# Performance work log

Hardware: AMD Instinct MI355X
Metric: run time of the kernel (lower is better)

Reference implementation:

```python
import jax, jax.numpy as jnp
import numpy as np

B, C_IN, T = 8, 1024, 4096
VQ_C, CODEBOOK, DS = 1024, 2048, 2


def setup_inputs() -> dict:
    key = jax.random.key(0)
    ks = jax.random.split(key, 6)
    return {
        "x": jax.random.normal(ks[0], (B, C_IN, T), jnp.float32),
        "x_mask": jnp.ones((B, 1, T), jnp.float32),
        "w_in": jax.random.normal(ks[1], (VQ_C, C_IN, DS), jnp.float32) * 0.02,
        "b_in": jnp.zeros((VQ_C,), jnp.float32),
        "embed": jax.random.normal(ks[2], (CODEBOOK, VQ_C), jnp.float32),
        "w_out": jax.random.normal(ks[3], (C_IN, VQ_C), jnp.float32) * 0.02,
        "b_out": jnp.zeros((C_IN,), jnp.float32),
    }


def reference(x, x_mask, w_in, b_in, embed, w_out, b_out):
    x_len = x.shape[2]
    ds = w_in.shape[-1]
    pad = (-x_len) % ds  # static under jit
    if pad:
        x = jnp.pad(x, ((0, 0), (0, 0), (0, pad)))
        x_mask = jnp.pad(x_mask, ((0, 0), (0, 0), (0, pad)))
    b, cin, tp = x.shape
    # conv_in: Conv1d(k=ds, stride=ds) == non-overlapping window contraction
    h = jnp.einsum('bcls,ocs->bol', x.reshape(b, cin, tp // ds, ds), w_in) + b_in[None, :, None]  # [B, D, L]
    tokens = h.transpose(0, 2, 1)  # [B, L, D]
    # euclidean codebook: ||t - e||^2 expanded (stable for argmin)
    d2 = (jnp.sum(tokens * tokens, -1, keepdims=True)
          - 2.0 * jnp.einsum('bld,nd->bln', tokens, embed)
          + jnp.sum(embed * embed, -1)[None, None, :])  # [B, L, N]
    idx = jnp.argmin(d2, axis=-1)  # [B, L]
    q = embed[idx]  # gather -> [B, L, D]
    # commitment loss (training-mode math; EMA codebook -> embed not a grad path)
    commit_loss = jnp.mean((jax.lax.stop_gradient(q) - tokens) ** 2)
    # straight-through estimator
    q_st = tokens + jax.lax.stop_gradient(q - tokens)
    q_cf = q_st.transpose(0, 2, 1)  # [B, D, L]
    # conv_out: nearest upsample x ds, then 1x1 conv
    up = jnp.repeat(q_cf, ds, axis=2)  # [B, D, Tp]
    out = jnp.einsum('bct,oc->bot', up, w_out) + b_out[None, :, None]
    out = out * x_mask
    return out[:, :, :x_len], commit_loss
```

## Files before the change

### kernel.cpp

```cpp
#include <hip/hip_runtime.h>

typedef _Float16 half8 __attribute__((ext_vector_type(8)));
typedef float f32x4 __attribute__((ext_vector_type(4)));

static constexpr int D = 1024;
static constexpr int NCODE = 2048;
static constexpr int MTOK = 16384;
static constexpr int KIN = 2048;
static constexpr int TLEN = 4096;
static constexpr int CAP = 2048;
#define TAU 0.4f

__device__ __forceinline__ void gload16(const void* g, void* l) {
  __builtin_amdgcn_global_load_lds(
      (const __attribute__((address_space(1))) void*)g,
      (__attribute__((address_space(3))) void*)l, 16, 0, 0);
}

#define SBAR()   asm volatile("s_barrier" ::: "memory")
#define WAITV6() asm volatile("s_waitcnt vmcnt(6)" ::: "memory")
#define WAITV4() asm volatile("s_waitcnt vmcnt(4)" ::: "memory")
#define WAITV3() asm volatile("s_waitcnt vmcnt(3)" ::: "memory")
#define WAITV0() asm volatile("s_waitcnt vmcnt(0)" ::: "memory")

__device__ __forceinline__ float key_to_f32(unsigned u) {
  unsigned bits = (u & 0x80000000u) ? (u & 0x7FFFFFFFu) : ~u;
  return __uint_as_float(bits);
}
__device__ __forceinline__ unsigned f32_to_key(float f) {
  unsigned ub = __float_as_uint(f);
  return (ub & 0x80000000u) ? ~ub : (ub | 0x80000000u);
}

__global__ __launch_bounds__(256) void k_pack_x(const float* __restrict__ x,
                                                _Float16* __restrict__ xh,
                                                _Float16* __restrict__ xl) {
  __shared__ float lds[32][65];
  const int tt0 = blockIdx.x * 64;
  const int cc0 = blockIdx.y * 32;
  const int b = blockIdx.z;
  const float* xb = x + ((size_t)b * D + cc0) * TLEN + tt0;
#pragma unroll
  for (int i = 0; i < 8; ++i) {
    int idx = threadIdx.x + i * 256;
    lds[idx >> 6][idx & 63] = xb[(size_t)(idx >> 6) * TLEN + (idx & 63)];
  }
  __syncthreads();
  const size_t mrow0 = (size_t)b * 2048 + (tt0 >> 1);
#pragma unroll
  for (int i = 0; i < 8; ++i) {
    int idx = threadIdx.x + i * 256;
    int r = idx >> 6, kk = idx & 63;
    float v = lds[kk >> 1][2 * r + (kk & 1)];
    _Float16 h = (_Float16)v;
    size_t off = (mrow0 + r) * (size_t)KIN + (size_t)cc0 * 2 + kk;
    xh[off] = h;
    xl[off] = (_Float16)(v - (float)h);
  }
}

__global__ __launch_bounds__(256) void k_split(const float* __restrict__ s,
                                               _Float16* __restrict__ hi,
                                               _Float16* __restrict__ lo, int n) {
  int i = blockIdx.x * 256 + threadIdx.x;
  if (i < n) {
    float v = s[i];
    _Float16 h = (_Float16)v;
    hi[i] = h;
    lo[i] = (_Float16)(v - (float)h);
  }
}

__global__ __launch_bounds__(256) void k_tohalf(const float* __restrict__ s,
                                                _Float16* __restrict__ hi, int n) {
  int i = blockIdx.x * 256 + threadIdx.x;
  if (i < n) hi[i] = (_Float16)s[i];
}

__global__ __launch_bounds__(256) void k_e2(const float* __restrict__ embed,
                                            float* __restrict__ e2c) {
  int row = blockIdx.x * 4 + (threadIdx.x >> 6);
  int lane = threadIdx.x & 63;
  const float* er = embed + (size_t)row * D;
  double s = 0.0;
  for (int i = lane; i < D; i += 64) { double v = er[i]; s += v * v; }
#pragma unroll
  for (int mk = 1; mk < 64; mk <<= 1) s += __shfl_xor(s, mk, 64);
  if (lane == 0) e2c[row] = (float)(s - 1024.0);
}

template <int KDIM, int LOG_GX>
__global__ __launch_bounds__(512, 2) void k_gemm_tok3(
    const _Float16* __restrict__ Ah_, const _Float16* __restrict__ Al_,
    const _Float16* __restrict__ Bh_, const _Float16* __restrict__ Bl_,
    const float* __restrict__ vec,
    _Float16* __restrict__ outh, _Float16* __restrict__ outl,
    float* __restrict__ t2) {
  __shared__ _Float16 lds[3 * 24576];
  const int nwg = gridDim.x;
  const int bid = blockIdx.x;
  const int q = nwg >> 3;
  const int b2 = (bid & 7) * q + (bid >> 3);
  const int n0 = (b2 & ((1 << LOG_GX) - 1)) * 128;
  const int m0 = (b2 >> LOG_GX) * 256;

  const int tid = threadIdx.x, lane = tid & 63, w = tid >> 6;
  const int wr = w >> 1, wc = w & 1, lr = lane & 15, lk = lane >> 4;
  constexpr int NT = KDIM / 32;

  const int cswz8 = (((lane & 3) ^ ((lane >> 3) & 3))) * 8;
  const int rswz8 = (lk ^ ((lr >> 1) & 3)) * 8;

  f32x4 acc[4][4] = {};
  half8 ahA[4], bhA[4], ahB[4], bhB[4], al[4], bl[4];

  auto stageA2 = [&](const _Float16* __restrict__ src, int k0, char* regionBase) {
    int slot0 = w * 64 + lane;
    gload16(src + (size_t)(m0 + (slot0 >> 2)) * KDIM + k0 + cswz8,
            regionBase + w * 1024);
    int slot1 = slot0 + 512;
    gload16(src + (size_t)(m0 + (slot1 >> 2)) * KDIM + k0 + cswz8,
            regionBase + w * 1024 + 8192);
  };
  auto stageB2 = [&](int k0, char* stageBase) {
    int slot = w * 64 + lane;
    size_t go = (size_t)(n0 + (slot >> 2)) * KDIM + k0 + cswz8;
    gload16(Bh_ + go, stageBase + 32768 + w * 1024);
    gload16(Bl_ + go, stageBase + 40960 + w * 1024);
  };
  auto stageAll = [&](int t, int c) {
    char* sb = (char*)lds + c * 49152;
    stageA2(Ah_, t * 32, sb);
    stageA2(Al_, t * 32, sb + 16384);
    stageB2(t * 32, sb);
  };

  int c0 = 0, c1 = 1, c2 = 2;
  stageAll(0, 0);
  stageAll(1, 1);
  WAITV6();
  SBAR();
#pragma unroll
  for (int f = 0; f < 4; ++f) {
    ahA[f] = *(const half8*)(lds + (wr * 64 + f * 16 + lr) * 32 + rswz8);
    bhA[f] = *(const half8*)(lds + 16384 + (wc * 64 + f * 16 + lr) * 32 + rswz8);
  }

  auto tile_body = [&](int t, half8 (&ahC)[4], half8 (&bhC)[4],
                       half8 (&ahN)[4], half8 (&bhN)[4]) {
    const _Float16* sb = lds + c0 * 24576;
    char* dstb = (char*)lds + c2 * 49152;
    const bool st = (t + 2) < NT;
    const int ks = (t + 2) * 32;

#pragma unroll
    for (int f = 0; f < 4; ++f)
      bl[f] = *(const half8*)(sb + 20480 + (wc * 64 + f * 16 + lr) * 32 + rswz8);
    if (st) stageA2(Ah_, ks, dstb);
    SBAR();
    __builtin_amdgcn_s_setprio(1);
#pragma unroll
    for (int fm = 0; fm < 4; ++fm)
#pragma unroll
      for (int fn = 0; fn < 4; ++fn)
        acc[fm][fn] = __builtin_amdgcn_mfma_f32_16x16x32_f16(ahC[fm], bhC[fn], acc[fm][fn], 0, 0, 0);
    __builtin_amdgcn_s_setprio(0);
    SBAR();

#pragma unroll
    for (int f = 0; f < 4; ++f)
      al[f] = *(const half8*)(sb + 8192 + (wr * 64 + f * 16 + lr) * 32 + rswz8);
    if (st) stageA2(Al_, ks, dstb + 16384);
    WAITV4();
    SBAR();
    __builtin_amdgcn_s_setprio(1);
#pragma unroll
    for (int fm = 0; fm < 4; ++fm)
#pragma unroll
      for (int fn = 0; fn < 4; ++fn)
        acc[fm][fn] = __builtin_amdgcn_mfma_f32_16x16x32_f16(ahC[fm], bl[fn], acc[fm][fn], 0, 0, 0);
    __builtin_amdgcn_s_setprio(0);
    SBAR();

    if (t + 1 < NT) {
      const _Float16* sb1 = lds + c1 * 24576;
#pragma unroll
      for (int f = 0; f < 4; ++f) {
        ahN[f] = *(const half8*)(sb1 + (wr * 64 + f * 16 + lr) * 32 + rswz8);
        bhN[f] = *(const half8*)(sb1 + 16384 + (wc * 64 + f * 16 + lr) * 32 + rswz8);
      }
    }
    if (st) stageB2(ks, dstb);
    SBAR();
    __builtin_amdgcn_s_setprio(1);
#pragma unroll
    for (int fm = 0; fm < 4; ++fm)
#pragma unroll
      for (int fn = 0; fn < 4; ++fn)
        acc[fm][fn] = __builtin_amdgcn_mfma_f32_16x16x32_f16(al[fm], bhC[fn], acc[fm][fn], 0, 0, 0);
    __builtin_amdgcn_s_setprio(0);
    if (st) { WAITV6(); } else if (t + 1 < NT) { WAITV0(); }
    SBAR();

    int tmp = c0; c0 = c1; c1 = c2; c2 = tmp;
  };

  for (int tt = 0; tt < NT; tt += 2) {
    tile_body(tt,     ahA, bhA, ahB, bhB);
    tile_body(tt + 1, ahB, bhB, ahA, bhA);
  }

#pragma unroll
  for (int fm = 0; fm < 4; ++fm) {
#pragma unroll
    for (int j = 0; j < 4; ++j) {
      int row = wr * 64 + fm * 16 + lk * 4 + j;
      size_t m = (size_t)m0 + row;
      float v2 = 0.f;
#pragma unroll
      for (int fn = 0; fn < 4; ++fn) {
        int col = n0 + wc * 64 + fn * 16 + lr;
        float v = acc[fm][fn][j] + vec[col];
        v2 += v * v;
        _Float16 h = (_Float16)v;
        outh[m * D + col] = h;
        outl[m * D + col] = (_Float16)(v - (float)h);
      }
#pragma unroll
      for (int mk = 1; mk < 16; mk <<= 1) v2 += __shfl_xor(v2, mk, 64);
      if (lr == 0) atomicAdd(&t2[m], v2);
    }
  }
}

__global__ __launch_bounds__(512, 4) void k_score1(
    const _Float16* __restrict__ Ah_, const _Float16* __restrict__ Bh_,
    const float* __restrict__ e2c,
    unsigned long long* __restrict__ skKey, float* __restrict__ skSnd) {
  __shared__ _Float16 lds[3 * 12288];
  const int nwg = gridDim.x, bid = blockIdx.x, q = nwg >> 3;
  const int b2 = (bid & 7) * q + (bid >> 3);
  const int nb = b2 & 15;
  const int n0 = nb * 128, m0 = (b2 >> 4) * 256;
  const int tid = threadIdx.x, lane = tid & 63, w = tid >> 6;
  const int wr = w >> 1, wc = w & 1, lr = lane & 15, lk = lane >> 4;
  constexpr int NT = D / 32;
  const int cswz8 = (((lane & 3) ^ ((lane >> 3) & 3))) * 8;
  const int rswz8 = (lk ^ ((lr >> 1) & 3)) * 8;

  f32x4 acc[4][4] = {};

  auto stage = [&](int t, int c) {
    char* sb = (char*)lds + c * 24576;
    const int k0 = t * 32;
    int slot0 = w * 64 + lane;
    gload16(Ah_ + (size_t)(m0 + (slot0 >> 2)) * D + k0 + cswz8, sb + w * 1024);
    int slot1 = slot0 + 512;
    gload16(Ah_ + (size_t)(m0 + (slot1 >> 2)) * D + k0 + cswz8, sb + w * 1024 + 8192);
    gload16(Bh_ + (size_t)(n0 + (slot0 >> 2)) * D + k0 + cswz8, sb + 16384 + w * 1024);
  };

  stage(0, 0);
  stage(1, 1);
  WAITV3();
  SBAR();

  int c0 = 0, c1 = 1, c2 = 2;
  for (int t = 0; t < NT; ++t) {
    const _Float16* sb = lds + c0 * 12288;
    half8 ah[4], bh[4];
#pragma unroll
    for (int f = 0; f < 4; ++f) {
      ah[f] = *(const half8*)(sb + (wr * 64 + f * 16 + lr) * 32 + rswz8);
      bh[f] = *(const half8*)(sb + 8192 + (wc * 64 + f * 16 + lr) * 32 + rswz8);
    }
    const bool st = (t + 2) < NT;
    if (st) stage(t + 2, c2);
    SBAR();
    __builtin_amdgcn_s_setprio(1);
#pragma unroll
    for (int fm = 0; fm < 4; ++fm)
#pragma unroll
      for (int fn = 0; fn < 4; ++fn)
        acc[fm][fn] = __builtin_amdgcn_mfma_f32_16x16x32_f16(ah[fm], bh[fn], acc[fm][fn], 0, 0, 0);
    __builtin_amdgcn_s_setprio(0);
    if (st) { WAITV3(); } else if (t + 1 < NT) { WAITV0(); }
    SBAR();
    int tmp = c0; c0 = c1; c1 = c2; c2 = tmp;
  }

#pragma unroll
  for (int fm = 0; fm < 4; ++fm) {
#pragma unroll
    for (int j = 0; j < 4; ++j) {
      int row = wr * 64 + fm * 16 + lk * 4 + j;
      size_t m = (size_t)m0 + row;
      float b1 = 3.4e38f, bb2 = 3.4e38f;
      int i1 = 0x7FFFFFFF;
#pragma unroll
      for (int fn = 0; fn < 4; ++fn) {
        int col = n0 + wc * 64 + fn * 16 + lr;
        float mv = e2c[col] - 2.0f * acc[fm][fn][j];
        if (mv < b1) { bb2 = b1; b1 = mv; i1 = col; }
        else if (mv < bb2) { bb2 = mv; }
      }
#pragma unroll
      for (int mk = 1; mk < 16; mk <<= 1) {
        float ob1 = __shfl_xor(b1, mk, 64);
        float ob2 = __shfl_xor(bb2, mk, 64);
        int oi = __shfl_xor(i1, mk, 64);
        if (ob1 < b1) { bb2 = fminf(b1, ob2); b1 = ob1; i1 = oi; }
        else { bb2 = fminf(bb2, ob1); }
      }
      if (lr == 0) {
        unsigned long long key = ((unsigned long long)f32_to_key(b1) << 32) | (unsigned)i1;
        skKey[m * 32 + nb * 2 + wc] = key;
        skSnd[m * 32 + nb * 2 + wc] = bb2;
      }
    }
  }
}

__global__ __launch_bounds__(256) void k_flag(const unsigned long long* __restrict__ skKey,
                                              const float* __restrict__ skSnd,
                                              unsigned long long* __restrict__ keys,
                                              int* __restrict__ list, int* __restrict__ counter) {
  int m = blockIdx.x * 256 + threadIdx.x;
  unsigned long long best = ~0ull;
  int bsl = 0;
#pragma unroll
  for (int sl = 0; sl < 32; ++sl) {
    unsigned long long k = skKey[(size_t)m * 32 + sl];
    if (k < best) { best = k; bsl = sl; }
  }
  float b1 = key_to_f32((unsigned)(best >> 32));
  float second = skSnd[(size_t)m * 32 + bsl];
#pragma unroll
  for (int sl = 0; sl < 32; ++sl) {
    if (sl != bsl) second = fminf(second, key_to_f32((unsigned)(skKey[(size_t)m * 32 + sl] >> 32)));
  }
  keys[m] = best;
  if (second - b1 < TAU) {
    int p = atomicAdd(counter, 1);
    if (p < CAP) list[p] = m;
  }
}

__global__ __launch_bounds__(256) void k_rescore(
    const _Float16* __restrict__ tokh, const _Float16* __restrict__ tokl,
    const _Float16* __restrict__ eh, const _Float16* __restrict__ el,
    const float* __restrict__ e2c, const int* __restrict__ list,
    const int* __restrict__ counter,
    unsigned long long* __restrict__ keys2) {
  const int count = min(counter[0], CAP);
  const int m0 = blockIdx.y * 128;
  if (m0 >= count) return;
  __shared__ _Float16 sAh[128 * 32], sAl[128 * 32], sBh[128 * 32], sBl[128 * 32];
  const int n0 = blockIdx.x * 128;
  const int tid = threadIdx.x, lane = tid & 63, w = tid >> 6;
  const int wr = w >> 1, wc = w & 1, lr = lane & 15, lk = lane >> 4;
  f32x4 acc[4][4] = {};

  const int g0 = w * 128 + lane, g1 = g0 + 64;
  const int rA0 = g0 >> 2, cA0 = g0 & 3, rA1 = g1 >> 2, cA1 = g1 & 3;
  const int lb0 = (w * 128) * 16, lb1 = (w * 128 + 64) * 16;
  const int tk0 = list[m0 + rA0], tk1 = list[m0 + rA1];

  for (int kt = 0; kt < D / 32; ++kt) {
    const int k0 = kt * 32;
    gload16(tokh + (size_t)tk0 * D + k0 + cA0 * 8, (char*)sAh + lb0);
    gload16(tokh + (size_t)tk1 * D + k0 + cA1 * 8, (char*)sAh + lb1);
    gload16(tokl + (size_t)tk0 * D + k0 + cA0 * 8, (char*)sAl + lb0);
    gload16(tokl + (size_t)tk1 * D + k0 + cA1 * 8, (char*)sAl + lb1);
    gload16(eh + (size_t)(n0 + rA0) * D + k0 + cA0 * 8, (char*)sBh + lb0);
    gload16(eh + (size_t)(n0 + rA1) * D + k0 + cA1 * 8, (char*)sBh + lb1);
    gload16(el + (size_t)(n0 + rA0) * D + k0 + cA0 * 8, (char*)sBl + lb0);
    gload16(el + (size_t)(n0 + rA1) * D + k0 + cA1 * 8, (char*)sBl + lb1);
    __syncthreads();
    half8 ah[4], al2[4], bh[4], bl2[4];
#pragma unroll
    for (int f = 0; f < 4; ++f) {
      ah[f]  = *(const half8*)(sAh + (wr * 64 + f * 16 + lr) * 32 + lk * 8);
      al2[f] = *(const half8*)(sAl + (wr * 64 + f * 16 + lr) * 32 + lk * 8);
      bh[f]  = *(const half8*)(sBh + (wc * 64 + f * 16 + lr) * 32 + lk * 8);
      bl2[f] = *(const half8*)(sBl + (wc * 64 + f * 16 + lr) * 32 + lk * 8);
    }
#pragma unroll
    for (int fm = 0; fm < 4; ++fm)
#pragma unroll
      for (int fn = 0; fn < 4; ++fn) {
        acc[fm][fn] = __builtin_amdgcn_mfma_f32_16x16x32_f16(ah[fm], bh[fn], acc[fm][fn], 0, 0, 0);
        acc[fm][fn] = __builtin_amdgcn_mfma_f32_16x16x32_f16(ah[fm], bl2[fn], acc[fm][fn], 0, 0, 0);
        acc[fm][fn] = __builtin_amdgcn_mfma_f32_16x16x32_f16(al2[fm], bh[fn], acc[fm][fn], 0, 0, 0);
      }
    __syncthreads();
  }
#pragma unroll
  for (int fm = 0; fm < 4; ++fm) {
#pragma unroll
    for (int j = 0; j < 4; ++j) {
      int row = wr * 64 + fm * 16 + lk * 4 + j;
      if (m0 + row >= count) continue;
      int tm = list[m0 + row];
      float best = 3.4e38f;
      int bidx = 0x7FFFFFFF;
#pragma unroll
      for (int fn = 0; fn < 4; ++fn) {
        int col = n0 + wc * 64 + fn * 16 + lr;
        float mv = e2c[col] - 2.0f * acc[fm][fn][j];
        if (mv < best) { best = mv; bidx = col; }
      }
#pragma unroll
      for (int mk = 1; mk < 16; mk <<= 1) {
        float ob = __shfl_xor(best, mk, 64);
        int oi = __shfl_xor(bidx, mk, 64);
        if (ob < best || (ob == best && oi < bidx)) { best = ob; bidx = oi; }
      }
      if (lr == 0) {
        unsigned long long key = ((unsigned long long)f32_to_key(best) << 32) | (unsigned)bidx;
        atomicMin(&keys2[tm], key);
      }
    }
  }
}

__global__ __launch_bounds__(256) void k_merge(unsigned long long* __restrict__ keys,
                                               const unsigned long long* __restrict__ keys2) {
  int m = blockIdx.x * 256 + threadIdx.x;
  unsigned long long k2 = keys2[m];
  if (k2 != ~0ull) keys[m] = k2;
}

__global__ __launch_bounds__(256) void k_gemm_out(
    const _Float16* __restrict__ eh, const unsigned long long* __restrict__ keys,
    const _Float16* __restrict__ woh, const float* __restrict__ b_out,
    const float* __restrict__ mask, float* __restrict__ out) {
  __shared__ _Float16 sA[128 * 32], sB[128 * 32];
  __shared__ float sC[32 * 129];
  const int n0 = blockIdx.x * 128, m0 = blockIdx.y * 128;
  const int tid = threadIdx.x, lane = tid & 63, w = tid >> 6;
  const int wr = w >> 1, wc = w & 1, lr = lane & 15, lk = lane >> 4;
  f32x4 acc[4][4] = {};

  const int g0 = w * 128 + lane, g1 = g0 + 64;
  const int rA0 = g0 >> 2, cA0 = g0 & 3, rA1 = g1 >> 2, cA1 = g1 & 3;
  const int lb0 = (w * 128) * 16, lb1 = (w * 128 + 64) * 16;
  const unsigned i0 = (unsigned)(keys[m0 + rA0] & 0xFFFFFFFFull);
  const unsigned i1 = (unsigned)(keys[m0 + rA1] & 0xFFFFFFFFull);
  const _Float16* srcA0 = eh + (size_t)i0 * D + cA0 * 8;
  const _Float16* srcA1 = eh + (size_t)i1 * D + cA1 * 8;

  for (int kt = 0; kt < D / 32; ++kt) {
    const int k0 = kt * 32;
    gload16(srcA0 + k0, (char*)sA + lb0);
    gload16(srcA1 + k0, (char*)sA + lb1);
    gload16(woh + (size_t)(n0 + rA0) * D + k0 + cA0 * 8, (char*)sB + lb0);
    gload16(woh + (size_t)(n0 + rA1) * D + k0 + cA1 * 8, (char*)sB + lb1);
    __syncthreads();
    half8 a[4], b[4];
#pragma unroll
    for (int f = 0; f < 4; ++f) {
      a[f] = *(const half8*)(sA + (wr * 64 + f * 16 + lr) * 32 + lk * 8);
      b[f] = *(const half8*)(sB + (wc * 64 + f * 16 + lr) * 32 + lk * 8);
    }
#pragma unroll
    for (int fm = 0; fm < 4; ++fm)
#pragma unroll
      for (int fn = 0; fn < 4; ++fn)
        acc[fm][fn] = __builtin_amdgcn_mfma_f32_16x16x32_f16(a[fm], b[fn], acc[fm][fn], 0, 0, 0);
    __syncthreads();
  }
  for (int ch = 0; ch < 4; ++ch) {
    __syncthreads();
    if (wr == (ch >> 1)) {
      int fb = (ch & 1) * 2;
#pragma unroll
      for (int f2 = 0; f2 < 2; ++f2) {
        int fm = fb + f2;
#pragma unroll
        for (int fn = 0; fn < 4; ++fn)
#pragma unroll
          for (int j = 0; j < 4; ++j) {
            int lrow = f2 * 16 + lk * 4 + j;
            int col = wc * 64 + fn * 16 + lr;
            sC[lrow * 129 + col] = acc[fm][fn][j] + b_out[n0 + col];
          }
      }
    }
    __syncthreads();
    const int mbase = m0 + ch * 32;
    const int b = mbase >> 11;
    const int l0 = mbase & 2047;
    const float mval = mask[(size_t)b * TLEN + 2 * l0 + lane];
    for (int oo = 0; oo < 32; ++oo) {
      int ocol = w * 32 + oo;
      float v = sC[(lane >> 1) * 129 + ocol];
      out[((size_t)(b * D + n0 + ocol)) * TLEN + 2 * l0 + lane] = v * mval;
    }
  }
}

__global__ __launch_bounds__(256) void k_loss(const unsigned long long* __restrict__ keys,
                                              const float* __restrict__ t2,
                                              double* __restrict__ acc) {
  int m = blockIdx.x * 256 + threadIdx.x;
  unsigned long long k = keys[m];
  float mval = key_to_f32((unsigned)(k >> 32));
  double c = (double)mval + 1024.0 + (double)t2[m];
#pragma unroll
  for (int mk = 1; mk < 64; mk <<= 1) c += __shfl_xor(c, mk, 64);
  __shared__ double part[4];
  if ((threadIdx.x & 63) == 0) part[threadIdx.x >> 6] = c;
  __syncthreads();
  if (threadIdx.x == 0) atomicAdd(acc, part[0] + part[1] + part[2] + part[3]);
}

__global__ void k_finalize(const double* __restrict__ acc, float* __restrict__ dst) {
  if (threadIdx.x == 0 && blockIdx.x == 0) *dst = (float)(*acc * (1.0 / 16777216.0));
}

extern "C" void kernel_launch(void* const* d_in, const int* in_sizes, int n_in,
                              void* d_out, int out_size, void* d_ws, size_t ws_size,
                              hipStream_t stream) {
  (void)in_sizes; (void)n_in; (void)out_size;
  const float* x      = (const float*)d_in[0];
  const float* xmask  = (const float*)d_in[1];
  const float* w_in   = (const float*)d_in[2];
  const float* b_in   = (const float*)d_in[3];
  const float* embed  = (const float*)d_in[4];
  const float* w_out  = (const float*)d_in[5];
  const float* b_out  = (const float*)d_in[6];
  float* out = (float*)d_out;

  _Float16* xh = (_Float16*)d_out;
  _Float16* xl = xh + (size_t)MTOK * KIN;

  char* p = (char*)d_ws;
  auto take = [&](size_t sz) { char* r = p; p += (sz + 255) & ~(size_t)255; return r; };
  _Float16* wh   = (_Float16*)take((size_t)D * KIN * 2);
  _Float16* wl   = (_Float16*)take((size_t)D * KIN * 2);
  _Float16* eh   = (_Float16*)take((size_t)NCODE * D * 2);
  _Float16* el   = (_Float16*)take((size_t)NCODE * D * 2);
  _Float16* woh  = (_Float16*)take((size_t)D * D * 2);
  float* e2c     = (float*)take((size_t)NCODE * 4);
  _Float16* tokh = (_Float16*)take((size_t)MTOK * D * 2);
  _Float16* tokl = (_Float16*)take((size_t)MTOK * D * 2);
  float* t2      = (float*)take((size_t)MTOK * 4);
  unsigned long long* keys  = (unsigned long long*)take((size_t)MTOK * 8);
  unsigned long long* keys2 = (unsigned long long*)take((size_t)MTOK * 8);
  unsigned long long* skKey = (unsigned long long*)take((size_t)MTOK * 32 * 8);
  float* skSnd   = (float*)take((size_t)MTOK * 32 * 4);
  int* list      = (int*)take((size_t)CAP * 4);
  int* counter   = (int*)take(256);
  double* lossacc = (double*)take(256);
  if ((size_t)(p - (char*)d_ws) > ws_size) return;

  hipMemsetAsync(keys2, 0xFF, (size_t)MTOK * 8, stream);
  hipMemsetAsync(t2, 0, (size_t)MTOK * 4, stream);
  hipMemsetAsync(list, 0, (size_t)CAP * 4, stream);
  hipMemsetAsync(counter, 0, 256, stream);
  hipMemsetAsync(lossacc, 0, 8, stream);

  k_pack_x<<<dim3(64, 32, 8), 256, 0, stream>>>(x, xh, xl);
  k_split<<<(D * KIN + 255) / 256, 256, 0, stream>>>(w_in, wh, wl, D * KIN);
  k_split<<<(NCODE * D + 255) / 256, 256, 0, stream>>>(embed, eh, el, NCODE * D);
  k_tohalf<<<(D * D + 255) / 256, 256, 0, stream>>>(w_out, woh, D * D);
  k_e2<<<NCODE / 4, 256, 0, stream>>>(embed, e2c);

  k_gemm_tok3<KIN, 3><<<512, 512, 0, stream>>>(xh, xl, wh, wl, b_in, tokh, tokl, t2);

  k_score1<<<1024, 512, 0, stream>>>(tokh, eh, e2c, skKey, skSnd);
  k_flag<<<MTOK / 256, 256, 0, stream>>>(skKey, skSnd, keys, list, counter);
  k_rescore<<<dim3(NCODE / 128, CAP / 128), 256, 0, stream>>>(tokh, tokl, eh, el, e2c, list, counter, keys2);
  k_merge<<<MTOK / 256, 256, 0, stream>>>(keys, keys2);

  k_gemm_out<<<dim3(D / 128, MTOK / 128), 256, 0, stream>>>(eh, keys, woh, b_out, xmask, out);

  k_loss<<<MTOK / 256, 256, 0, stream>>>(keys, t2, lossacc);
  k_finalize<<<1, 64, 0, stream>>>(lossacc, out + (size_t)MTOK * KIN);
}
```

Measured before the change: 496.4 us.

## Use single-fp16 token GEMM and recompute split-precision tokens only for flagged rows

The conv_in GEMM now uses only the high fp16 halves (one MFMA pass instead of three) and writes fp16 tokens. The split-precision tokens are recomputed by a new gather GEMM, but only for the ambiguous tokens that k_flag puts on the rescore list. The token and scoring GEMMs now share one templated kernel with 256x256 tiles. This cuts the dominant GEMM work and the stores of the low-half tokens. In exchange the squared norms and first-pass scores come from less precise tokens, and an extra gather kernel is added.

After: 452.2 us. -8.9%, faster.

```diff
diff --git a/kernel.cpp b/kernel.cpp
--- a/kernel.cpp
+++ b/kernel.cpp
@@ -18,9 +18,7 @@
 }
 
 #define SBAR()   asm volatile("s_barrier" ::: "memory")
-#define WAITV6() asm volatile("s_waitcnt vmcnt(6)" ::: "memory")
 #define WAITV4() asm volatile("s_waitcnt vmcnt(4)" ::: "memory")
-#define WAITV3() asm volatile("s_waitcnt vmcnt(3)" ::: "memory")
 #define WAITV0() asm volatile("s_waitcnt vmcnt(0)" ::: "memory")
 
 __device__ __forceinline__ float key_to_f32(unsigned u) {
@@ -89,233 +87,113 @@
   if (lane == 0) e2c[row] = (float)(s - 1024.0);
 }
 
-template <int KDIM, int LOG_GX>
-__global__ __launch_bounds__(512, 2) void k_gemm_tok3(
-    const _Float16* __restrict__ Ah_, const _Float16* __restrict__ Al_,
-    const _Float16* __restrict__ Bh_, const _Float16* __restrict__ Bl_,
+template <int KDIM, int LOG_GX, int MODE>
+__global__ __launch_bounds__(512, 2) void k_gemm_hh(
+    const _Float16* __restrict__ Ah_, const _Float16* __restrict__ Bh_,
     const float* __restrict__ vec,
-    _Float16* __restrict__ outh, _Float16* __restrict__ outl,
-    float* __restrict__ t2) {
-  __shared__ _Float16 lds[3 * 24576];
-  const int nwg = gridDim.x;
-  const int bid = blockIdx.x;
-  const int q = nwg >> 3;
+    _Float16* __restrict__ outh, float* __restrict__ t2,
+    unsigned long long* __restrict__ skKey, float* __restrict__ skSnd) {
+  __shared__ _Float16 lds[3 * 16384];
+  const int nwg = gridDim.x, bid = blockIdx.x, q = nwg >> 3;
   const int b2 = (bid & 7) * q + (bid >> 3);
-  const int n0 = (b2 & ((1 << LOG_GX) - 1)) * 128;
-  const int m0 = (b2 >> LOG_GX) * 256;
-
+  const int nb = b2 & ((1 << LOG_GX) - 1);
+  const int n0 = nb * 256, m0 = (b2 >> LOG_GX) * 256;
   const int tid = threadIdx.x, lane = tid & 63, w = tid >> 6;
-  const int wr = w >> 1, wc = w & 1, lr = lane & 15, lk = lane >> 4;
+  const int wr = w >> 2, wc = w & 3, lr = lane & 15, lk = lane >> 4;
   constexpr int NT = KDIM / 32;
-
   const int cswz8 = (((lane & 3) ^ ((lane >> 3) & 3))) * 8;
   const int rswz8 = (lk ^ ((lr >> 1) & 3)) * 8;
 
-  f32x4 acc[4][4] = {};
-  half8 ahA[4], bhA[4], ahB[4], bhB[4], al[4], bl[4];
-
-  auto stageA2 = [&](const _Float16* __restrict__ src, int k0, char* regionBase) {
-    int slot0 = w * 64 + lane;
-    gload16(src + (size_t)(m0 + (slot0 >> 2)) * KDIM + k0 + cswz8,
-            regionBase + w * 1024);
-    int slot1 = slot0 + 512;
-    gload16(src + (size_t)(m0 + (slot1 >> 2)) * KDIM + k0 + cswz8,
-            regionBase + w * 1024 + 8192);
-  };
-  auto stageB2 = [&](int k0, char* stageBase) {
-    int slot = w * 64 + lane;
-    size_t go = (size_t)(n0 + (slot >> 2)) * KDIM + k0 + cswz8;
-    gload16(Bh_ + go, stageBase + 32768 + w * 1024);
-    gload16(Bl_ + go, stageBase + 40960 + w * 1024);
-  };
-  auto stageAll = [&](int t, int c) {
-    char* sb = (char*)lds + c * 49152;
-    stageA2(Ah_, t * 32, sb);
-    stageA2(Al_, t * 32, sb + 16384);
-    stageB2(t * 32, sb);
-  };
-
-  int c0 = 0, c1 = 1, c2 = 2;
-  stageAll(0, 0);
-  stageAll(1, 1);
-  WAITV6();
-  SBAR();
-#pragma unroll
-  for (int f = 0; f < 4; ++f) {
-    ahA[f] = *(const half8*)(lds + (wr * 64 + f * 16 + lr) * 32 + rswz8);
-    bhA[f] = *(const half8*)(lds + 16384 + (wc * 64 + f * 16 + lr) * 32 + rswz8);
-  }
-
-  auto tile_body = [&](int t, half8 (&ahC)[4], half8 (&bhC)[4],
-                       half8 (&ahN)[4], half8 (&bhN)[4]) {
-    const _Float16* sb = lds + c0 * 24576;
-    char* dstb = (char*)lds + c2 * 49152;
-    const bool st = (t + 2) < NT;
-    const int ks = (t + 2) * 32;
-
-#pragma unroll
-    for (int f = 0; f < 4; ++f)
-      bl[f] = *(const half8*)(sb + 20480 + (wc * 64 + f * 16 + lr) * 32 + rswz8);
-    if (st) stageA2(Ah_, ks, dstb);
-    SBAR();
-    __builtin_amdgcn_s_setprio(1);
-#pragma unroll
-    for (int fm = 0; fm < 4; ++fm)
-#pragma unroll
-      for (int fn = 0; fn < 4; ++fn)
-        acc[fm][fn] = __builtin_amdgcn_mfma_f32_16x16x32_f16(ahC[fm], bhC[fn], acc[fm][fn], 0, 0, 0);
-    __builtin_amdgcn_s_setprio(0);
-    SBAR();
-
-#pragma unroll
-    for (int f = 0; f < 4; ++f)
-      al[f] = *(const half8*)(sb + 8192 + (wr * 64 + f * 16 + lr) * 32 + rswz8);
-    if (st) stageA2(Al_, ks, dstb + 16384);
-    WAITV4();
-    SBAR();
-    __builtin_amdgcn_s_setprio(1);
-#pragma unroll
-    for (int fm = 0; fm < 4; ++fm)
-#pragma unroll
-      for (int fn = 0; fn < 4; ++fn)
-        acc[fm][fn] = __builtin_amdgcn_mfma_f32_16x16x32_f16(ahC[fm], bl[fn], acc[fm][fn], 0, 0, 0);
-    __builtin_amdgcn_s_setprio(0);
-    SBAR();
-
-    if (t + 1 < NT) {
-      const _Float16* sb1 = lds + c1 * 24576;
-#pragma unroll
-      for (int f = 0; f < 4; ++f) {
-        ahN[f] = *(const half8*)(sb1 + (wr * 64 + f * 16 + lr) * 32 + rswz8);
-        bhN[f] = *(const half8*)(sb1 + 16384 + (wc * 64 + f * 16 + lr) * 32 + rswz8);
-      }
-    }
-    if (st) stageB2(ks, dstb);
-    SBAR();
-    __builtin_amdgcn_s_setprio(1);
-#pragma unroll
-    for (int fm = 0; fm < 4; ++fm)
-#pragma unroll
-      for (int fn = 0; fn < 4; ++fn)
-        acc[fm][fn] = __builtin_amdgcn_mfma_f32_16x16x32_f16(al[fm], bhC[fn], acc[fm][fn], 0, 0, 0);
-    __builtin_amdgcn_s_setprio(0);
-    if (st) { WAITV6(); } else if (t + 1 < NT) { WAITV0(); }
-    SBAR();
-
-    int tmp = c0; c0 = c1; c1 = c2; c2 = tmp;
-  };
-
-  for (int tt = 0; tt < NT; tt += 2) {
-    tile_body(tt,     ahA, bhA, ahB, bhB);
-    tile_body(tt + 1, ahB, bhB, ahA, bhA);
-  }
-
-#pragma unroll
-  for (int fm = 0; fm < 4; ++fm) {
-#pragma unroll
-    for (int j = 0; j < 4; ++j) {
-      int row = wr * 64 + fm * 16 + lk * 4 + j;
-      size_t m = (size_t)m0 + row;
-      float v2 = 0.f;
-#pragma unroll
-      for (int fn = 0; fn < 4; ++fn) {
-        int col = n0 + wc * 64 + fn * 16 + lr;
-        float v = acc[fm][fn][j] + vec[col];
-        v2 += v * v;
-        _Float16 h = (_Float16)v;
-        outh[m * D + col] = h;
-        outl[m * D + col] = (_Float16)(v - (float)h);
-      }
-#pragma unroll
-      for (int mk = 1; mk < 16; mk <<= 1) v2 += __shfl_xor(v2, mk, 64);
-      if (lr == 0) atomicAdd(&t2[m], v2);
-    }
-  }
-}
-
-__global__ __launch_bounds__(512, 4) void k_score1(
-    const _Float16* __restrict__ Ah_, const _Float16* __restrict__ Bh_,
-    const float* __restrict__ e2c,
-    unsigned long long* __restrict__ skKey, float* __restrict__ skSnd) {
-  __shared__ _Float16 lds[3 * 12288];
-  const int nwg = gridDim.x, bid = blockIdx.x, q = nwg >> 3;
-  const int b2 = (bid & 7) * q + (bid >> 3);
-  const int nb = b2 & 15;
-  const int n0 = nb * 128, m0 = (b2 >> 4) * 256;
-  const int tid = threadIdx.x, lane = tid & 63, w = tid >> 6;
-  const int wr = w >> 1, wc = w & 1, lr = lane & 15, lk = lane >> 4;
-  constexpr int NT = D / 32;
-  const int cswz8 = (((lane & 3) ^ ((lane >> 3) & 3))) * 8;
-  const int rswz8 = (lk ^ ((lr >> 1) & 3)) * 8;
-
-  f32x4 acc[4][4] = {};
+  f32x4 acc[8][4] = {};
 
   auto stage = [&](int t, int c) {
-    char* sb = (char*)lds + c * 24576;
+    char* sb = (char*)(lds + c * 16384);
     const int k0 = t * 32;
-    int slot0 = w * 64 + lane;
-    gload16(Ah_ + (size_t)(m0 + (slot0 >> 2)) * D + k0 + cswz8, sb + w * 1024);
-    int slot1 = slot0 + 512;
-    gload16(Ah_ + (size_t)(m0 + (slot1 >> 2)) * D + k0 + cswz8, sb + w * 1024 + 8192);
-    gload16(Bh_ + (size_t)(n0 + (slot0 >> 2)) * D + k0 + cswz8, sb + 16384 + w * 1024);
+    const int r0 = (w * 64 + lane) >> 2;
+    gload16(Ah_ + (size_t)(m0 + r0) * KDIM + k0 + cswz8, sb + w * 1024);
+    gload16(Ah_ + (size_t)(m0 + 128 + r0) * KDIM + k0 + cswz8, sb + w * 1024 + 8192);
+    gload16(Bh_ + (size_t)(n0 + r0) * KDIM + k0 + cswz8, sb + 16384 + w * 1024);
+    gload16(Bh_ + (size_t)(n0 + 128 + r0) * KDIM + k0 + cswz8, sb + 16384 + w * 1024 + 8192);
   };
 
   stage(0, 0);
   stage(1, 1);
-  WAITV3();
+  WAITV4();
   SBAR();
 
   int c0 = 0, c1 = 1, c2 = 2;
   for (int t = 0; t < NT; ++t) {
-    const _Float16* sb = lds + c0 * 12288;
-    half8 ah[4], bh[4];
-#pragma unroll
-    for (int f = 0; f < 4; ++f) {
-      ah[f] = *(const half8*)(sb + (wr * 64 + f * 16 + lr) * 32 + rswz8);
-      bh[f] = *(const half8*)(sb + 8192 + (wc * 64 + f * 16 + lr) * 32 + rswz8);
-    }
     const bool st = (t + 2) < NT;
     if (st) stage(t + 2, c2);
-    SBAR();
+    const _Float16* sb = lds + c0 * 16384;
+    half8 ah[8], bh[4];
+#pragma unroll
+    for (int f = 0; f < 8; ++f)
+      ah[f] = *(const half8*)(sb + (wr * 128 + f * 16 + lr) * 32 + rswz8);
+#pragma unroll
+    for (int f = 0; f < 4; ++f)
+      bh[f] = *(const half8*)(sb + 8192 + (wc * 64 + f * 16 + lr) * 32 + rswz8);
     __builtin_amdgcn_s_setprio(1);
 #pragma unroll
-    for (int fm = 0; fm < 4; ++fm)
+    for (int fm = 0; fm < 8; ++fm)
 #pragma unroll
       for (int fn = 0; fn < 4; ++fn)
         acc[fm][fn] = __builtin_amdgcn_mfma_f32_16x16x32_f16(ah[fm], bh[fn], acc[fm][fn], 0, 0, 0);
     __builtin_amdgcn_s_setprio(0);
-    if (st) { WAITV3(); } else if (t + 1 < NT) { WAITV0(); }
+    if (st) { WAITV4(); } else if (t + 1 < NT) { WAITV0(); }
     SBAR();
     int tmp = c0; c0 = c1; c1 = c2; c2 = tmp;
   }
 
-#pragma unroll
-  for (int fm = 0; fm < 4; ++fm) {
-#pragma unroll
-    for (int j = 0; j < 4; ++j) {
-      int row = wr * 64 + fm * 16 + lk * 4 + j;
-      size_t m = (size_t)m0 + row;
-      float b1 = 3.4e38f, bb2 = 3.4e38f;
-      int i1 = 0x7FFFFFFF;
-#pragma unroll
-      for (int fn = 0; fn < 4; ++fn) {
-        int col = n0 + wc * 64 + fn * 16 + lr;
-        float mv = e2c[col] - 2.0f * acc[fm][fn][j];
-        if (mv < b1) { bb2 = b1; b1 = mv; i1 = col; }
-        else if (mv < bb2) { bb2 = mv; }
-      }
-#pragma unroll
-      for (int mk = 1; mk < 16; mk <<= 1) {
-        float ob1 = __shfl_xor(b1, mk, 64);
-        float ob2 = __shfl_xor(bb2, mk, 64);
-        int oi = __shfl_xor(i1, mk, 64);
-        if (ob1 < b1) { bb2 = fminf(b1, ob2); b1 = ob1; i1 = oi; }
-        else { bb2 = fminf(bb2, ob1); }
-      }
-      if (lr == 0) {
-        unsigned long long key = ((unsigned long long)f32_to_key(b1) << 32) | (unsigned)i1;
-        skKey[m * 32 + nb * 2 + wc] = key;
-        skSnd[m * 32 + nb * 2 + wc] = bb2;
+  if constexpr (MODE == 0) {
+#pragma unroll
+    for (int fm = 0; fm < 8; ++fm) {
+#pragma unroll
+      for (int j = 0; j < 4; ++j) {
+        int row = wr * 128 + fm * 16 + lk * 4 + j;
+        size_t m = (size_t)m0 + row;
+        float v2 = 0.f;
+#pragma unroll
+        for (int fn = 0; fn < 4; ++fn) {
+          int col = n0 + wc * 64 + fn * 16 + lr;
+          float v = acc[fm][fn][j] + vec[col];
+          v2 += v * v;
+          outh[m * (size_t)D + col] = (_Float16)v;
+        }
+#pragma unroll
+        for (int mk = 1; mk < 16; mk <<= 1) v2 += __shfl_xor(v2, mk, 64);
+        if (lr == 0) atomicAdd(&t2[m], v2);
+      }
+    }
+  } else {
+#pragma unroll
+    for (int fm = 0; fm < 8; ++fm) {
+#pragma unroll
+      for (int j = 0; j < 4; ++j) {
+        int row = wr * 128 + fm * 16 + lk * 4 + j;
+        size_t m = (size_t)m0 + row;
+        float b1 = 3.4e38f, bb2 = 3.4e38f;
+        int i1 = 0x7FFFFFFF;
+#pragma unroll
+        for (int fn = 0; fn < 4; ++fn) {
+          int col = n0 + wc * 64 + fn * 16 + lr;
+          float mv = vec[col] - 2.0f * acc[fm][fn][j];
+          if (mv < b1) { bb2 = b1; b1 = mv; i1 = col; }
+          else if (mv < bb2) { bb2 = mv; }
+        }
+#pragma unroll
+        for (int mk = 1; mk < 16; mk <<= 1) {
+          float ob1 = __shfl_xor(b1, mk, 64);
+          float ob2 = __shfl_xor(bb2, mk, 64);
+          int oi = __shfl_xor(i1, mk, 64);
+          if (ob1 < b1) { bb2 = fminf(b1, ob2); b1 = ob1; i1 = oi; }
+          else { bb2 = fminf(bb2, ob1); }
+        }
+        if (lr == 0) {
+          unsigned long long key = ((unsigned long long)f32_to_key(b1) << 32) | (unsigned)i1;
+          skKey[m * 32 + nb * 4 + wc] = key;
+          skSnd[m * 32 + nb * 4 + wc] = bb2;
+        }
       }
     }
   }
@@ -346,8 +224,76 @@
   }
 }
 
+__global__ __launch_bounds__(256) void k_tok_fix(
+    const _Float16* __restrict__ xh, const _Float16* __restrict__ xl,
+    const _Float16* __restrict__ wh, const _Float16* __restrict__ wl,
+    const float* __restrict__ b_in, const int* __restrict__ list,
+    const int* __restrict__ counter,
+    _Float16* __restrict__ tokh2, _Float16* __restrict__ tokl2) {
+  const int count = min(counter[0], CAP);
+  const int m0 = blockIdx.y * 128;
+  if (m0 >= count) return;
+  __shared__ _Float16 sAh[128 * 32], sAl[128 * 32], sBh[128 * 32], sBl[128 * 32];
+  const int n0 = blockIdx.x * 128;
+  const int tid = threadIdx.x, lane = tid & 63, w = tid >> 6;
+  const int wr = w >> 1, wc = w & 1, lr = lane & 15, lk = lane >> 4;
+  f32x4 acc[4][4] = {};
+
+  const int g0 = w * 128 + lane, g1 = g0 + 64;
+  const int rA0 = g0 >> 2, cA0 = g0 & 3, rA1 = g1 >> 2, cA1 = g1 & 3;
+  const int lb0 = (w * 128) * 16, lb1 = (w * 128 + 64) * 16;
+  const int tk0 = list[min(m0 + rA0, count - 1)];
+  const int tk1 = list[min(m0 + rA1, count - 1)];
+
+  for (int kt = 0; kt < KIN / 32; ++kt) {
+    const int k0 = kt * 32;
+    gload16(xh + (size_t)tk0 * KIN + k0 + cA0 * 8, (char*)sAh + lb0);
+    gload16(xh + (size_t)tk1 * KIN + k0 + cA1 * 8, (char*)sAh + lb1);
+    gload16(xl + (size_t)tk0 * KIN + k0 + cA0 * 8, (char*)sAl + lb0);
+    gload16(xl + (size_t)tk1 * KIN + k0 + cA1 * 8, (char*)sAl + lb1);
+    gload16(wh + (size_t)(n0 + rA0) * KIN + k0 + cA0 * 8, (char*)sBh + lb0);
+    gload16(wh + (size_t)(n0 + rA1) * KIN + k0 + cA1 * 8, (char*)sBh + lb1);
+    gload16(wl + (size_t)(n0 + rA0) * KIN + k0 + cA0 * 8, (char*)sBl + lb0);
+    gload16(wl + (size_t)(n0 + rA1) * KIN + k0 + cA1 * 8, (char*)sBl + lb1);
+    __syncthreads();
+    half8 ah[4], al2[4], bh[4], bl2[4];
+#pragma unroll
+    for (int f = 0; f < 4; ++f) {
+      ah[f]  = *(const half8*)(sAh + (wr * 64 + f * 16 + lr) * 32 + lk * 8);
+      al2[f] = *(const half8*)(sAl + (wr * 64 + f * 16 + lr) * 32 + lk * 8);
+      bh[f]  = *(const half8*)(sBh + (wc * 64 + f * 16 + lr) * 32 + lk * 8);
+      bl2[f] = *(const half8*)(sBl + (wc * 64 + f * 16 + lr) * 32 + lk * 8);
+    }
+#pragma unroll
+    for (int fm = 0; fm < 4; ++fm)
+#pragma unroll
+      for (int fn = 0; fn < 4; ++fn) {
+        acc[fm][fn] = __builtin_amdgcn_mfma_f32_16x16x32_f16(ah[fm], bh[fn], acc[fm][fn], 0, 0, 0);
+        acc[fm][fn] = __builtin_amdgcn_mfma_f32_16x16x32_f16(ah[fm], bl2[fn], acc[fm][fn], 0, 0, 0);
+        acc[fm][fn] = __builtin_amdgcn_mfma_f32_16x16x32_f16(al2[fm], bh[fn], acc[fm][fn], 0, 0, 0);
+      }
+    __syncthreads();
+  }
+#pragma unroll
+  for (int fm = 0; fm < 4; ++fm) {
+#pragma unroll
+    for (int j = 0; j < 4; ++j) {
+      int row = wr * 64 + fm * 16 + lk * 4 + j;
+      if (m0 + row >= count) continue;
+#pragma unroll
+      for (int fn = 0; fn < 4; ++fn) {
+        int col = n0 + wc * 64 + fn * 16 + lr;
+        float v = acc[fm][fn][j] + b_in[col];
+        _Float16 h = (_Float16)v;
+        tokh2[(size_t)(m0 + row) * D + col] = h;
+        tokl2[(size_t)(m0 + row) * D + col] = (_Float16)(v - (float)h);
+      }
+    }
+  }
+}
+
 __global__ __launch_bounds__(256) void k_rescore(
-    const _Float16* __restrict__ tokh, const _Float16* __restrict__ tokl,
+    const _Float16* __restrict__ tokh2, const _Float16* __restrict__ tokl2,
     const _Float16* __restrict__ eh, const _Float16* __restrict__ el,
     const float* __restrict__ e2c, const int* __restrict__ list,
     const int* __restrict__ counter,
@@ -364,14 +310,13 @@
   const int g0 = w * 128 + lane, g1 = g0 + 64;
   const int rA0 = g0 >> 2, cA0 = g0 & 3, rA1 = g1 >> 2, cA1 = g1 & 3;
   const int lb0 = (w * 128) * 16, lb1 = (w * 128 + 64) * 16;
-  const int tk0 = list[m0 + rA0], tk1 = list[m0 + rA1];
 
   for (int kt = 0; kt < D / 32; ++kt) {
     const int k0 = kt * 32;
-    gload16(tokh + (size_t)tk0 * D + k0 + cA0 * 8, (char*)sAh + lb0);
-    gload16(tokh + (size_t)tk1 * D + k0 + cA1 * 8, (char*)sAh + lb1);
-    gload16(tokl + (size_t)tk0 * D + k0 + cA0 * 8, (char*)sAl + lb0);
-    gload16(tokl + (size_t)tk1 * D + k0 + cA1 * 8, (char*)sAl + lb1);
+    gload16(tokh2 + (size_t)(m0 + rA0) * D + k0 + cA0 * 8, (char*)sAh + lb0);
+    gload16(tokh2 + (size_t)(m0 + rA1) * D + k0 + cA1 * 8, (char*)sAh + lb1);
+    gload16(tokl2 + (size_t)(m0 + rA0) * D + k0 + cA0 * 8, (char*)sAl + lb0);
+    gload16(tokl2 + (size_t)(m0 + rA1) * D + k0 + cA1 * 8, (char*)sAl + lb1);
     gload16(eh + (size_t)(n0 + rA0) * D + k0 + cA0 * 8, (char*)sBh + lb0);
     gload16(eh + (size_t)(n0 + rA1) * D + k0 + cA1 * 8, (char*)sBh + lb1);
     gload16(el + (size_t)(n0 + rA0) * D + k0 + cA0 * 8, (char*)sBl + lb0);
@@ -537,21 +482,22 @@
 
   char* p = (char*)d_ws;
   auto take = [&](size_t sz) { char* r = p; p += (sz + 255) & ~(size_t)255; return r; };
-  _Float16* wh   = (_Float16*)take((size_t)D * KIN * 2);
-  _Float16* wl   = (_Float16*)take((size_t)D * KIN * 2);
-  _Float16* eh   = (_Float16*)take((size_t)NCODE * D * 2);
-  _Float16* el   = (_Float16*)take((size_t)NCODE * D * 2);
-  _Float16* woh  = (_Float16*)take((size_t)D * D * 2);
-  float* e2c     = (float*)take((size_t)NCODE * 4);
-  _Float16* tokh = (_Float16*)take((size_t)MTOK * D * 2);
-  _Float16* tokl = (_Float16*)take((size_t)MTOK * D * 2);
-  float* t2      = (float*)take((size_t)MTOK * 4);
+  _Float16* wh    = (_Float16*)take((size_t)D * KIN * 2);
+  _Float16* wl    = (_Float16*)take((size_t)D * KIN * 2);
+  _Float16* eh    = (_Float16*)take((size_t)NCODE * D * 2);
+  _Float16* el    = (_Float16*)take((size_t)NCODE * D * 2);
+  _Float16* woh   = (_Float16*)take((size_t)D * D * 2);
+  float* e2c      = (float*)take((size_t)NCODE * 4);
+  _Float16* tokh  = (_Float16*)take((size_t)MTOK * D * 2);
+  _Float16* tokh2 = (_Float16*)take((size_t)CAP * D * 2);
+  _Float16* tokl2 = (_Float16*)take((size_t)CAP * D * 2);
+  float* t2       = (float*)take((size_t)MTOK * 4);
   unsigned long long* keys  = (unsigned long long*)take((size_t)MTOK * 8);
   unsigned long long* keys2 = (unsigned long long*)take((size_t)MTOK * 8);
   unsigned long long* skKey = (unsigned long long*)take((size_t)MTOK * 32 * 8);
-  float* skSnd   = (float*)take((size_t)MTOK * 32 * 4);
-  int* list      = (int*)take((size_t)CAP * 4);
-  int* counter   = (int*)take(256);
+  float* skSnd    = (float*)take((size_t)MTOK * 32 * 4);
+  int* list       = (int*)take((size_t)CAP * 4);
+  int* counter    = (int*)take(256);
   double* lossacc = (double*)take(256);
   if ((size_t)(p - (char*)d_ws) > ws_size) return;
 
@@ -567,11 +513,11 @@
   k_tohalf<<<(D * D + 255) / 256, 256, 0, stream>>>(w_out, woh, D * D);
   k_e2<<<NCODE / 4, 256, 0, stream>>>(embed, e2c);
 
-  k_gemm_tok3<KIN, 3><<<512, 512, 0, stream>>>(xh, xl, wh, wl, b_in, tokh, tokl, t2);
-
-  k_score1<<<1024, 512, 0, stream>>>(tokh, eh, e2c, skKey, skSnd);
+  k_gemm_hh<KIN, 2, 0><<<256, 512, 0, stream>>>(xh, wh, b_in, tokh, t2, nullptr, nullptr);
+  k_gemm_hh<D, 3, 1><<<512, 512, 0, stream>>>(tokh, eh, e2c, nullptr, nullptr, skKey, skSnd);
   k_flag<<<MTOK / 256, 256, 0, stream>>>(skKey, skSnd, keys, list, counter);
-  k_rescore<<<dim3(NCODE / 128, CAP / 128), 256, 0, stream>>>(tokh, tokl, eh, el, e2c, list, counter, keys2);
+  k_tok_fix<<<dim3(D / 128, CAP / 128), 256, 0, stream>>>(xh, xl, wh, wl, b_in, list, counter, tokh2, tokl2);
+  k_rescore<<<dim3(NCODE / 128, CAP / 128), 256, 0, stream>>>(tokh2, tokl2, eh, el, e2c, list, counter, keys2);
   k_merge<<<MTOK / 256, 256, 0, stream>>>(keys, keys2);
 
   k_gemm_out<<<dim3(D / 128, MTOK / 128), 256, 0, stream>>>(eh, keys, woh, b_out, xmask, out);
```
